# Optimization experiments

Hardware: AMD Instinct MI355X
Metric: run time of the kernel (lower is better)

Reference implementation:

```python
import jax, jax.numpy as jnp
import numpy as np

N = 3600      # nodes (pinned by h0/c0 shape in the torch module)
H = 512       # lstm_hidden
PES = 588     # pes feature width (LSTM input size)
PROT = 384    # protein feature width
OC = 256      # out_channels
E = 230400    # edges (avg degree 64)


def _lstm_cell(x, h, c, wih, whh, bih, bhh):
    # single-timestep PyTorch LSTM cell; gate order i, f, g, o
    g = x @ wih.T + h @ whh.T + bih + bhh
    i, f, gg, o = jnp.split(g, 4, axis=-1)
    c2 = jax.nn.sigmoid(f) * c + jax.nn.sigmoid(i) * jnp.tanh(gg)
    return jax.nn.sigmoid(o) * jnp.tanh(c2)


def _gcn(x, rows, cols, norm, W, b):
    # PyG GCNConv: X' = D^{-1/2}(A+I)D^{-1/2} X W + b
    xw = x @ W
    return jax.ops.segment_sum(xw[rows] * norm[:, None], cols, num_segments=N) + b


def setup_inputs() -> dict:
    key = jax.random.key(0)
    ks = jax.random.split(key, 24)
    s = 0.05
    d = {
        "x": jax.random.normal(ks[0], (N, PES + PROT), jnp.float32),
        "edge_index": jax.random.randint(ks[1], (2, E), 0, N),
        "h0": jax.random.normal(ks[2], (4, N, H), jnp.float32),
        "c0": jax.random.normal(ks[3], (4, N, H), jnp.float32),
    }
    ins = [PES, PES, 2 * H, 2 * H]
    names = ["l0f", "l0b", "l1f", "l1b"]
    for i, (nm, di) in enumerate(zip(names, ins)):
        d["wih" + nm] = jax.random.normal(ks[4 + 4 * i], (4 * H, di), jnp.float32) * s
        d["whh" + nm] = jax.random.normal(ks[5 + 4 * i], (4 * H, H), jnp.float32) * s
        d["bih" + nm] = jnp.zeros((4 * H,), jnp.float32)
        d["bhh" + nm] = jnp.zeros((4 * H,), jnp.float32)
    d["W1"] = jax.random.normal(ks[20], (PROT + 2 * H, 2 * OC), jnp.float32) * s
    d["b1"] = jnp.zeros((2 * OC,), jnp.float32)
    d["W2"] = jax.random.normal(ks[21], (2 * OC, OC), jnp.float32) * s
    d["b2"] = jnp.zeros((OC,), jnp.float32)
    return d


def reference(x, edge_index, h0, c0,
              wihl0f, whhl0f, bihl0f, bhhl0f,
              wihl0b, whhl0b, bihl0b, bhhl0b,
              wihl1f, whhl1f, bihl1f, bhhl1f,
              wihl1b, whhl1b, bihl1b, bhhl1b,
              W1, b1, W2, b2):
    pes = x[:, :PES]
    prot = x[:, PES:]
    # BiLSTM over seq_len=1: one cell step per direction per layer
    hf = _lstm_cell(pes, h0[0], c0[0], wihl0f, whhl0f, bihl0f, bhhl0f)
    hb = _lstm_cell(pes, h0[1], c0[1], wihl0b, whhl0b, bihl0b, bhhl0b)
    x1 = jnp.concatenate([hf, hb], axis=1)
    hf2 = _lstm_cell(x1, h0[2], c0[2], wihl1f, whhl1f, bihl1f, bhhl1f)
    hb2 = _lstm_cell(x1, h0[3], c0[3], wihl1b, whhl1b, bihl1b, bhhl1b)
    x_p = jnp.concatenate([hf2, hb2], axis=1) / 100.0
    feat = jnp.concatenate([prot, x_p], axis=1)  # dropout is identity in eval
    # add self-loops, symmetric normalization
    loop = jnp.arange(N)
    rows = jnp.concatenate([edge_index[0], loop])
    cols = jnp.concatenate([edge_index[1], loop])
    deg = jax.ops.segment_sum(jnp.ones_like(rows, jnp.float32), cols, num_segments=N)
    dinv = jax.lax.rsqrt(deg)  # deg >= 1 because of self-loops
    norm = dinv[rows] * dinv[cols]
    h1 = jax.nn.relu(_gcn(feat, rows, cols, norm, W1, b1))
    return _gcn(h1, rows, cols, norm, W2, b2)
```

## Files before the change

kernel.cpp:

```cpp
#include <hip/hip_runtime.h>
#include <hip/hip_bf16.h>

#define NN 3600
#define MP 3712
#define KADJ 3616
#define NH (3600*512)
#define EE 230400
#define NKT0 9
#define NKT1 12

typedef __hip_bfloat16 bf16;
typedef __bf16 bf16x8 __attribute__((ext_vector_type(8)));
typedef float f32x4 __attribute__((ext_vector_type(4)));
typedef int i32x8 __attribute__((ext_vector_type(8)));
typedef unsigned char u8x16 __attribute__((ext_vector_type(16)));

typedef __attribute__((address_space(1))) void as1v;
typedef __attribute__((address_space(3))) void as3v;

__device__ __forceinline__ void glds16(void* lds, const void* g) {
  __builtin_amdgcn_global_load_lds((as1v*)(void*)g, (as3v*)lds, 16, 0, 0);
}

__device__ __forceinline__ float sigm(float v) { return 1.0f / (1.0f + expf(-v)); }

__device__ __forceinline__ unsigned char f2fp8(float f) {
  return (unsigned char)(__builtin_amdgcn_cvt_pk_fp8_f32(f, 0.f, 0, false) & 0xff);
}

__device__ __forceinline__ unsigned short f2bf_bits(float f) {
  __hip_bfloat16 h = __float2bfloat16(f);
  return *reinterpret_cast<unsigned short*>(&h);
}
__device__ __forceinline__ float bf_bits2f(unsigned short u) {
  __hip_bfloat16 h; *reinterpret_cast<unsigned short*>(&h) = u;
  return __bfloat162float(h);
}

template<int MODE>
__global__ __launch_bounds__(256) void gemm_lstm8(
    const unsigned char* __restrict__ Axf, const unsigned char* __restrict__ Ahf,
    const unsigned char* __restrict__ Bf,
    const float* __restrict__ c0f, const float* __restrict__ bihf,
    const float* __restrict__ bhhf,
    const unsigned char* __restrict__ Axb, const unsigned char* __restrict__ Ahb,
    const unsigned char* __restrict__ Bb,
    const float* __restrict__ c0b, const float* __restrict__ bihb,
    const float* __restrict__ bhhb,
    void* __restrict__ dst1,
    int nktx, int nkt, int hx)
{
  __shared__ alignas(16) unsigned char smem[65536];
  const int hid = (int)blockIdx.y * 32 + (int)blockIdx.x;
  const int xcd = hid & 7, idx = hid >> 3;
  int bx, by;
  if (idx < 112) { bx = (xcd & 3) * 8 + (idx & 7); by = (xcd >> 2) * 14 + (idx >> 3); }
  else { int k = idx - 112; bx = (xcd & 3) * 8 + k * 2 + (xcd >> 2); by = 28; }
  const bool back = bx >= hx;
  const unsigned char* Ax = back ? Axb : Axf;
  const unsigned char* Ah = back ? Ahb : Ahf;
  const unsigned char* B  = back ? Bb  : Bf;
  const float* c0  = back ? c0b : c0f;
  const float* bih = back ? bihb : bihf;
  const float* bhh = back ? bhhb : bhhf;
  const int t = threadIdx.x, w = t >> 6, l = t & 63;
  const int nblk = back ? bx - hx : bx;
  const unsigned char* gA  = Ax + (((size_t)by * nktx) << 14) + t*16;
  const unsigned char* gAh = Ah + (((size_t)by * (nkt - nktx)) << 14) + t*16;
  const unsigned char* gB  = B  + (((size_t)nblk * nkt) << 14) + t*16;
  const int wm = (w>>1)*64, wn = (w&1)*64;
  const int kb = l >> 4;
  const int aoff = kb*4096 + (wm + (l&15))*32;
  const int boff = 16384 + kb*4096 + (wn + (l&15))*32;
  f32x4 acc[4][4] = {};

  auto STAGE = [&](int buf, int kt) {
    unsigned char* lA = smem + buf*32768 + w*1024;
    unsigned char* lB = smem + buf*32768 + 16384 + w*1024;
    const unsigned char* srcA = (kt < nktx) ? gA + ((size_t)kt << 14)
                                            : gAh + ((size_t)(kt - nktx) << 14);
    const size_t ko = (size_t)kt << 14;
    glds16(lA,          srcA);
    glds16(lA + 4096,   srcA + 4096);
    glds16(lA + 8192,   srcA + 8192);
    glds16(lA + 12288,  srcA + 12288);
    glds16(lB,          gB + ko);
    glds16(lB + 4096,   gB + ko + 4096);
    glds16(lB + 8192,   gB + ko + 8192);
    glds16(lB + 12288,  gB + ko + 12288);
  };

  STAGE(0, 0);
  STAGE(1, 1);
  int cur = 0;
  for (int kt = 0; kt < nkt; ++kt) {
    if (kt + 1 < nkt) asm volatile("s_waitcnt vmcnt(8)" ::: "memory");
    else              asm volatile("s_waitcnt vmcnt(0)" ::: "memory");
    __builtin_amdgcn_sched_barrier(0);
    __builtin_amdgcn_s_barrier();
    __builtin_amdgcn_sched_barrier(0);
    const unsigned char* base = smem + cur*32768;
    i32x8 av[4], bv[4];
#pragma unroll
    for (int mi = 0; mi < 4; ++mi) av[mi] = *(const i32x8*)(base + aoff + mi*512);
#pragma unroll
    for (int ni = 0; ni < 4; ++ni) bv[ni] = *(const i32x8*)(base + boff + ni*512);
#pragma unroll
    for (int mi = 0; mi < 4; ++mi)
#pragma unroll
      for (int ni = 0; ni < 4; ++ni)
        acc[mi][ni] = __builtin_amdgcn_mfma_scale_f32_16x16x128_f8f6f4(
            av[mi], bv[ni], acc[mi][ni], 0, 0, 0, 127, 0, 127);
    __builtin_amdgcn_sched_barrier(0);
    __builtin_amdgcn_s_barrier();
    __builtin_amdgcn_sched_barrier(0);
    if (kt + 2 < nkt) STAGE(cur, kt + 2);
    cur ^= 1;
  }
  const int jh = (((nblk << 7) + wn) >> 2) + (l & 15);
  const float bI = bih[jh]        + bhh[jh];
  const float bF = bih[512 + jh]  + bhh[512 + jh];
  const float bG = bih[1024 + jh] + bhh[1024 + jh];
  const float bO = bih[1536 + jh] + bhh[1536 + jh];
  const int crow = (by << 7) + wm + ((l>>4)<<2);
  const int kk = (back ? 512 : 0) + jh;
  const size_t kpart = ((size_t)(kk >> 7) << 14) + ((size_t)((kk >> 5) & 3) << 12) + (kk & 31);
  const int colOff = back ? 896 : 384;
#pragma unroll
  for (int mi = 0; mi < 4; ++mi)
#pragma unroll
    for (int jr = 0; jr < 4; ++jr) {
      const int n = crow + mi*16 + jr;
      if (n < NN) {
        const float gi = acc[mi][0][jr] + bI;
        const float gf = acc[mi][1][jr] + bF;
        const float gg = acc[mi][2][jr] + bG;
        const float go = acc[mi][3][jr] + bO;
        const float c2 = sigm(gf) * c0[(size_t)n*512 + jh] + sigm(gi) * tanhf(gg);
        const float h  = sigm(go) * tanhf(c2);
        if (MODE == 0) {
          const size_t off = (((size_t)(n >> 7) * 8) << 14) + kpart + ((size_t)(n & 127) << 5);
          ((unsigned char*)dst1)[off] = f2fp8(h);
        } else {
          ((bf16*)dst1)[(size_t)n*1408 + colOff + jh] = __float2bfloat16(h * 0.01f);
        }
      }
    }
}

__global__ __launch_bounds__(256) void gemm_bt_sk(const bf16* __restrict__ A,
                                                  const bf16* __restrict__ B,
                                                  float* __restrict__ Cp,
                                                  int Kp, int ldc, int ksteps)
{
  __shared__ alignas(16) char smem[32768];
  const int t = threadIdx.x, w = t >> 6, l = t & 63;
  const int mbase = blockIdx.y << 7, nbase = blockIdx.x << 7;
  const int total = Kp >> 5;
  const int kstart = blockIdx.z * ksteps;
  int steps = total - kstart; if (steps > ksteps) steps = ksteps;
  const size_t ldb = (size_t)Kp * 2;
  const char* gA = (const char*)A + (size_t)(mbase + w*16 + (l>>2)) * ldb
                   + (size_t)((l&3)*16) + (size_t)kstart*64;
  const char* gB = (const char*)B + (size_t)(nbase + w*16 + (l>>2)) * ldb
                   + (size_t)((l&3)*16) + (size_t)kstart*64;
  const int wm = (w>>1)*64, wn = (w&1)*64;
  const int aoff = (wm + (l&15))*64 + (l>>4)*16;
  const int boff = 8192 + (wn + (l&15))*64 + (l>>4)*16;
  f32x4 acc[4][4] = {};
  const size_t chunk = ldb * 64;

  auto STAGE = [&](int buf, int kt) {
    char* lA = smem + buf*16384 + w*1024;
    char* lB = smem + buf*16384 + 8192 + w*1024;
    const size_t ko = (size_t)kt * 64;
    glds16(lA,        gA + ko);
    glds16(lA + 4096, gA + ko + chunk);
    glds16(lB,        gB + ko);
    glds16(lB + 4096, gB + ko + chunk);
  };

  STAGE(0, 0);
  if (steps > 1) STAGE(1, 1);
  int cur = 0;
  for (int kt = 0; kt < steps; ++kt) {
    if (kt + 1 < steps) asm volatile("s_waitcnt vmcnt(4)" ::: "memory");
    else                asm volatile("s_waitcnt vmcnt(0)" ::: "memory");
    __builtin_amdgcn_sched_barrier(0);
    __builtin_amdgcn_s_barrier();
    __builtin_amdgcn_sched_barrier(0);
    const char* base = smem + cur*16384;
    bf16x8 av[4], bv[4];
#pragma unroll
    for (int mi = 0; mi < 4; ++mi) av[mi] = *(const bf16x8*)(base + aoff + mi*1024);
#pragma unroll
    for (int ni = 0; ni < 4; ++ni) bv[ni] = *(const bf16x8*)(base + boff + ni*1024);
#pragma unroll
    for (int mi = 0; mi < 4; ++mi)
#pragma unroll
      for (int ni = 0; ni < 4; ++ni)
        acc[mi][ni] = __builtin_amdgcn_mfma_f32_16x16x32_bf16(av[mi], bv[ni], acc[mi][ni], 0, 0, 0);
    __builtin_amdgcn_sched_barrier(0);
    __builtin_amdgcn_s_barrier();
    __builtin_amdgcn_sched_barrier(0);
    if (kt + 2 < steps) STAGE(cur, kt + 2);
    cur ^= 1;
  }
  float* Cz = Cp + (size_t)blockIdx.z * ((size_t)(gridDim.y << 7) * ldc);
  const int crow = mbase + wm + ((l>>4)<<2);
  const int ccol = nbase + wn + (l&15);
#pragma unroll
  for (int mi = 0; mi < 4; ++mi)
#pragma unroll
    for (int ni = 0; ni < 4; ++ni) {
      float* cp = Cz + (size_t)(crow + mi*16)*ldc + (ccol + ni*16);
#pragma unroll
      for (int j = 0; j < 4; ++j) cp[(size_t)j*ldc] = acc[mi][ni][j];
    }
}

__global__ void reduce_bf_pad(const float* __restrict__ p, bf16* __restrict__ dst, int Z)
{
  int k = blockIdx.x*256 + threadIdx.x;
  int r = blockIdx.y;
  if (k >= KADJ) return;
  const size_t psz = (size_t)gridDim.y * MP;
  float s = 0.f;
  if (k < NN)
    for (int z = 0; z < Z; ++z) s += p[(size_t)z*psz + (size_t)r*MP + k];
  dst[(size_t)r*KADJ + k] = __float2bfloat16(s);
}

__global__ void reduce_relu_bf(const float* __restrict__ p, const float* __restrict__ b,
                               bf16* __restrict__ dst)
{
  int idx = blockIdx.x*256 + threadIdx.x;
  int f = idx & 511;
  float s = b[f];
#pragma unroll
  for (int z = 0; z < 4; ++z) s += p[(size_t)z*MP*512 + idx];
  dst[idx] = __float2bfloat16(fmaxf(s, 0.f));
}

__global__ void reduce_bias_out(const float* __restrict__ p, const float* __restrict__ b,
                                float* __restrict__ out)
{
  int idx = blockIdx.x*256 + threadIdx.x;
  if (idx >= NN*256) return;
  int f = idx & 255;
  float s = b[f];
#pragma unroll
  for (int z = 0; z < 8; ++z) s += p[(size_t)z*MP*256 + idx];
  out[idx] = s;
}

__global__ void pack_B8_all(const float* __restrict__ wih0f, const float* __restrict__ whh0f,
                            const float* __restrict__ wih0b, const float* __restrict__ whh0b,
                            const float* __restrict__ wih1f, const float* __restrict__ whh1f,
                            const float* __restrict__ wih1b, const float* __restrict__ whh1b,
                            unsigned char* __restrict__ B0f, unsigned char* __restrict__ B0b,
                            unsigned char* __restrict__ B1f, unsigned char* __restrict__ B1b)
{
  const int z = blockIdx.z;
  const float* wih; const float* whh; unsigned char* dst; int kx, nkt;
  if      (z == 0) { wih = wih0f; whh = whh0f; dst = B0f; kx = 588;  nkt = NKT0; }
  else if (z == 1) { wih = wih0b; whh = whh0b; dst = B0b; kx = 588;  nkt = NKT0; }
  else if (z == 2) { wih = wih1f; whh = whh1f; dst = B1f; kx = 1024; nkt = NKT1; }
  else             { wih = wih1b; whh = whh1b; dst = B1b; kx = 1024; nkt = NKT1; }
  if ((int)blockIdx.x >= nkt*4) return;
  const int kt = blockIdx.x >> 2, kbId = blockIdx.x & 3;
  const int t = threadIdx.x;
  const int r = t >> 1, kio = (t & 1) << 4;
  const int R = ((int)blockIdx.y << 7) + r;
  const int src = (((R >> 4) & 3) << 9) + ((R >> 6) << 4) + (R & 15);
  const int kbase = kt*128 + kbId*32 + kio;
  u8x16 v;
#pragma unroll
  for (int i = 0; i < 16; ++i) {
    const int k = kbase + i;
    float f = 0.f;
    if (k < kx) f = wih[(size_t)src*kx + k];
    else if (k < kx + 512) f = whh[(size_t)src*512 + (k - kx)];
    v[i] = f2fp8(f);
  }
  *(u8x16*)(dst + (((size_t)blockIdx.y*nkt + kt) << 14) + (kbId << 12) + (r << 5) + kio) = v;
}

__global__ void pack_A8_all(const float* __restrict__ x, const float* __restrict__ h0,
                            unsigned char* __restrict__ a0f, unsigned char* __restrict__ a0b,
                            unsigned char* __restrict__ ahf, unsigned char* __restrict__ ahb)
{
  const int z = blockIdx.z;
  const int t = threadIdx.x;
  const int r = t >> 1, kio = (t & 1) << 4;
  const int n = ((int)blockIdx.y << 7) + r;
  if (z < 2) {
    const int kt = blockIdx.x >> 2, kbId = blockIdx.x & 3;
    const int kbase = kt*128 + kbId*32 + kio;
    const float* hsrc = h0 + (size_t)z * NH;
    u8x16 v;
#pragma unroll
    for (int i = 0; i < 16; ++i) {
      const int k = kbase + i;
      float f = 0.f;
      if (n < NN) {
        if (k < 588) f = x[(size_t)n*972 + k];
        else if (k < 1100) f = hsrc[(size_t)n*512 + (k - 588)];
      }
      v[i] = f2fp8(f);
    }
    unsigned char* dst = z ? a0b : a0f;
    *(u8x16*)(dst + (((size_t)blockIdx.y*NKT0 + kt) << 14) + (kbId << 12) + (r << 5) + kio) = v;
  } else {
    if ((int)blockIdx.x >= 16) return;
    const int ktl = blockIdx.x >> 2, kbId = blockIdx.x & 3;
    const int kbase = ktl*128 + kbId*32 + kio;
    const float* hsrc = h0 + (size_t)(z) * NH;
    u8x16 v;
#pragma unroll
    for (int i = 0; i < 16; ++i) {
      const int k = kbase + i;
      float f = (n < NN) ? hsrc[(size_t)n*512 + k] : 0.f;
      v[i] = f2fp8(f);
    }
    unsigned char* dst = (z == 3) ? ahb : ahf;
    *(u8x16*)(dst + (((size_t)blockIdx.y*4 + ktl) << 14) + (kbId << 12) + (r << 5) + kio) = v;
  }
}

__global__ void pack_BT_all(const float* __restrict__ W1, bf16* __restrict__ BW1,
                            const float* __restrict__ W2, bf16* __restrict__ BW2)
{
  const int z = blockIdx.z;
  const float* W; bf16* dst; int Nc, K, nx, ny;
  if (z == 0) { W = W1; dst = BW1; Nc = 512; K = 1408; nx = 6; ny = 512; }
  else        { W = W2; dst = BW2; Nc = 256; K = 512;  nx = 2; ny = 256; }
  if ((int)blockIdx.x >= nx || (int)blockIdx.y >= ny) return;
  int k = blockIdx.x*256 + threadIdx.x;
  int n = blockIdx.y;
  if (k >= K) return;
  dst[(size_t)n*K + k] = __float2bfloat16(W[(size_t)k*Nc + n]);
}

__global__ void pack_prot(const float* __restrict__ x, bf16* __restrict__ afeat)
{
  int k = blockIdx.x*256 + threadIdx.x;
  int n = blockIdx.y;
  if (k >= 384) return;
  float v = (n < NN) ? x[(size_t)n*972 + 588 + k] : 0.f;
  afeat[(size_t)n*1408 + k] = __float2bfloat16(v);
}

__global__ void deg_count(const int* __restrict__ ecols, int* __restrict__ deg)
{
  int e = blockIdx.x*256 + threadIdx.x;
  if (e < EE) atomicAdd(&deg[ecols[e]], 1);
}

__global__ void calc_dinv(const int* __restrict__ deg, float* __restrict__ dinv)
{
  int n = blockIdx.x*256 + threadIdx.x;
  if (n < NN) dinv[n] = 1.0f / sqrtf((float)(deg[n] + 1));
}

__global__ void adj_scatter_bf(const int* __restrict__ er, const int* __restrict__ ec,
                               const float* __restrict__ dinv,
                               unsigned int* __restrict__ adjw)
{
  int e = blockIdx.x*256 + threadIdx.x;
  int r, c; float v;
  if (e < EE)            { r = er[e]; c = ec[e]; v = dinv[r]*dinv[c]; }
  else if (e < EE + NN)  { r = c = e - EE; float d = dinv[r]; v = d*d; }
  else return;
  unsigned int* p = adjw + ((size_t)c*KADJ + r) / 2;
  const bool hi = (r & 1) != 0;
  unsigned int old = *p, assumed;
  do {
    assumed = old;
    unsigned short h = hi ? (unsigned short)(assumed >> 16)
                          : (unsigned short)(assumed & 0xffffu);
    unsigned short nh = f2bf_bits(bf_bits2f(h) + v);
    unsigned int nw = hi ? ((assumed & 0x0000ffffu) | ((unsigned int)nh << 16))
                         : ((assumed & 0xffff0000u) | (unsigned int)nh);
    if (nw == assumed) break;
    old = atomicCAS(p, assumed, nw);
  } while (old != assumed);
}

#define OFF_DEG   ((size_t)0)
#define OFF_DINV  ((size_t)16384)
#define OFF_BW2   ((size_t)32768)
#define OFF_B0F   ((size_t)294912)
#define OFF_B0B   ((size_t)4882432)
#define OFF_B1F   ((size_t)9469952)
#define OFF_B1B   ((size_t)15761408)
#define OFF_BW1   ((size_t)22052864)
#define OFF_A0F   ((size_t)23494656)
#define OFF_A0B   ((size_t)31809536)
#define OFF_A1X   ((size_t)40124416)
#define OFF_A1HF  ((size_t)43925504)
#define OFF_A1HB  ((size_t)45826048)
#define OFF_G     ((size_t)62930944)
#define OFF_AFEAT OFF_A0F
#define OFF_XW1P  OFF_G
#define OFF_XWT1B OFF_B0F
#define OFF_ADJB  ((size_t)4194304)
#define OFF_H1P   ((size_t)40124416)
#define OFF_H1    ((size_t)70533120)
#define OFF_XW2P  ((size_t)74334208)
#define OFF_XWT2B ((size_t)89538560)
#define OFF_O2P   ((size_t)40124416)

extern "C" void kernel_launch(void* const* d_in, const int* in_sizes, int n_in,
                              void* d_out, int out_size, void* d_ws, size_t ws_size,
                              hipStream_t stream)
{
  const float* x    = (const float*)d_in[0];
  const int*   ei   = (const int*)d_in[1];
  const float* h0   = (const float*)d_in[2];
  const float* c0   = (const float*)d_in[3];
  const float* wih0f = (const float*)d_in[4];
  const float* whh0f = (const float*)d_in[5];
  const float* bih0f = (const float*)d_in[6];
  const float* bhh0f = (const float*)d_in[7];
  const float* wih0b = (const float*)d_in[8];
  const float* whh0b = (const float*)d_in[9];
  const float* bih0b = (const float*)d_in[10];
  const float* bhh0b = (const float*)d_in[11];
  const float* wih1f = (const float*)d_in[12];
  const float* whh1f = (const float*)d_in[13];
  const float* bih1f = (const float*)d_in[14];
  const float* bhh1f = (const float*)d_in[15];
  const float* wih1b = (const float*)d_in[16];
  const float* whh1b = (const float*)d_in[17];
  const float* bih1b = (const float*)d_in[18];
  const float* bhh1b = (const float*)d_in[19];
  const float* W1 = (const float*)d_in[20];
  const float* b1 = (const float*)d_in[21];
  const float* W2 = (const float*)d_in[22];
  const float* b2 = (const float*)d_in[23];

  char* ws = (char*)d_ws;
  int*   deg  = (int*)(ws + OFF_DEG);
  float* dinv = (float*)(ws + OFF_DINV);
  unsigned char* B0f8 = (unsigned char*)(ws + OFF_B0F);
  unsigned char* B0b8 = (unsigned char*)(ws + OFF_B0B);
  unsigned char* B1f8 = (unsigned char*)(ws + OFF_B1F);
  unsigned char* B1b8 = (unsigned char*)(ws + OFF_B1B);
  bf16* BW1 = (bf16*)(ws + OFF_BW1);
  bf16* BW2 = (bf16*)(ws + OFF_BW2);
  unsigned char* A0f8 = (unsigned char*)(ws + OFF_A0F);
  unsigned char* A0b8 = (unsigned char*)(ws + OFF_A0B);
  unsigned char* A1X8 = (unsigned char*)(ws + OFF_A1X);
  unsigned char* A1HF = (unsigned char*)(ws + OFF_A1HF);
  unsigned char* A1HB = (unsigned char*)(ws + OFF_A1HB);
  bf16* Afeat = (bf16*)(ws + OFF_AFEAT);
  float* xw1p  = (float*)(ws + OFF_XW1P);
  bf16*  xwt1b = (bf16*)(ws + OFF_XWT1B);
  bf16*  adjb  = (bf16*)(ws + OFF_ADJB);
  float* h1p   = (float*)(ws + OFF_H1P);
  bf16*  h1bf  = (bf16*)(ws + OFF_H1);
  float* xw2p  = (float*)(ws + OFF_XW2P);
  bf16*  xwt2b = (bf16*)(ws + OFF_XWT2B);
  float* o2p   = (float*)(ws + OFF_O2P);
  float* outp = (float*)d_out;

  hipMemsetAsync(deg, 0, (size_t)NN*4, stream);
  deg_count<<<dim3((EE+255)/256), 256, 0, stream>>>(ei + EE, deg);
  calc_dinv<<<dim3(15), 256, 0, stream>>>(deg, dinv);

  pack_B8_all<<<dim3(NKT1*4, 16, 4), 256, 0, stream>>>(
      wih0f, whh0f, wih0b, whh0b, wih1f, whh1f, wih1b, whh1b,
      B0f8, B0b8, B1f8, B1b8);
  pack_BT_all<<<dim3(6, 512, 2), 256, 0, stream>>>(W1, BW1, W2, BW2);

  pack_A8_all<<<dim3(NKT0*4, 29, 4), 256, 0, stream>>>(x, h0, A0f8, A0b8, A1HF, A1HB);

  gemm_lstm8<0><<<dim3(32, 29), 256, 0, stream>>>(
      A0f8, A0f8, B0f8, c0,              bih0f, bhh0f,
      A0b8, A0b8, B0b8, c0 + (size_t)NH, bih0b, bhh0b,
      A1X8, NKT0, NKT0, 16);

  pack_prot<<<dim3(2, MP), 256, 0, stream>>>(x, Afeat);

  gemm_lstm8<1><<<dim3(32, 29), 256, 0, stream>>>(
      A1X8, A1HF, B1f8, c0 + (size_t)2*NH, bih1f, bhh1f,
      A1X8, A1HB, B1b8, c0 + (size_t)3*NH, bih1b, bhh1b,
      Afeat, 8, NKT1, 16);

  gemm_bt_sk<<<dim3(29, 4, 4), 256, 0, stream>>>(BW1, Afeat, xw1p, 1408, MP, 11);
  reduce_bf_pad<<<dim3(15, 512), 256, 0, stream>>>(xw1p, xwt1b, 4);

  hipMemsetAsync(adjb, 0, (size_t)MP*KADJ*2, stream);
  adj_scatter_bf<<<dim3((EE+NN+255)/256), 256, 0, stream>>>(
      ei, ei + EE, dinv, (unsigned int*)adjb);

  gemm_bt_sk<<<dim3(4, 29, 4), 256, 0, stream>>>(adjb, xwt1b, h1p, KADJ, 512, 29);
  reduce_relu_bf<<<dim3(MP*512/256), 256, 0, stream>>>(h1p, b1, h1bf);

  gemm_bt_sk<<<dim3(29, 2, 4), 256, 0, stream>>>(BW2, h1bf, xw2p, 512, MP, 4);
  reduce_bf_pad<<<dim3(15, 256), 256, 0, stream>>>(xw2p, xwt2b, 4);

  gemm_bt_sk<<<dim3(2, 29, 8), 256, 0, stream>>>(adjb, xwt2b, o2p, KADJ, 256, 15);
  reduce_bias_out<<<dim3(3600), 256, 0, stream>>>(o2p, b2, outp);
}
```

Before: 297.0 us.

## Enlarge LSTM fp8 GEMM tiles to 256x256 with 512 threads and interleaved prefetch

The fused LSTM gate GEMM moves from 128x128 tiles with 256 threads to 256x256 tiles with 512 threads and 128KB of double-buffered LDS. Each wave now computes 4x8 MFMA tiles, and the next k-tile's global-to-LDS loads are interleaved with the MFMA groups, using s_setprio to favour the math. The grid shrinks to 240 blocks with a new XCD swizzle, and the packed A buffers are padded to 30 row blocks. The aim is more data reuse per loaded byte and better load/compute overlap. The cost is higher register and LDS pressure, which limits occupancy to one block per CU, and more barriers per k-step.

```diff
diff --git a/kernel.cpp b/kernel.cpp
--- a/kernel.cpp
+++ b/kernel.cpp
@@ -38,7 +38,7 @@
 }
 
 template<int MODE>
-__global__ __launch_bounds__(256) void gemm_lstm8(
+__global__ __launch_bounds__(512) void gemm_lstm8(
     const unsigned char* __restrict__ Axf, const unsigned char* __restrict__ Ahf,
     const unsigned char* __restrict__ Bf,
     const float* __restrict__ c0f, const float* __restrict__ bihf,
@@ -50,12 +50,10 @@
     void* __restrict__ dst1,
     int nktx, int nkt, int hx)
 {
-  __shared__ alignas(16) unsigned char smem[65536];
-  const int hid = (int)blockIdx.y * 32 + (int)blockIdx.x;
-  const int xcd = hid & 7, idx = hid >> 3;
-  int bx, by;
-  if (idx < 112) { bx = (xcd & 3) * 8 + (idx & 7); by = (xcd >> 2) * 14 + (idx >> 3); }
-  else { int k = idx - 112; bx = (xcd & 3) * 8 + k * 2 + (xcd >> 2); by = 28; }
+  __shared__ alignas(16) unsigned char smem[131072];
+  const int hid = (int)blockIdx.y * 16 + (int)blockIdx.x;
+  const int swz = (hid & 7) * 30 + (hid >> 3);
+  const int bx = swz & 15, by = swz >> 4;
   const bool back = bx >= hx;
   const unsigned char* Ax = back ? Axb : Axf;
   const unsigned char* Ah = back ? Ahb : Ahf;
@@ -64,88 +62,108 @@
   const float* bih = back ? bihb : bihf;
   const float* bhh = back ? bhhb : bhhf;
   const int t = threadIdx.x, w = t >> 6, l = t & 63;
+  const int wr = w >> 1, wc = w & 1;
   const int nblk = back ? bx - hx : bx;
-  const unsigned char* gA  = Ax + (((size_t)by * nktx) << 14) + t*16;
-  const unsigned char* gAh = Ah + (((size_t)by * (nkt - nktx)) << 14) + t*16;
-  const unsigned char* gB  = B  + (((size_t)nblk * nkt) << 14) + t*16;
-  const int wm = (w>>1)*64, wn = (w&1)*64;
+  const int nkth = nkt - nktx;
+  const unsigned char* gAx0 = Ax + (((size_t)(2*by)   * nktx) << 14);
+  const unsigned char* gAx1 = Ax + (((size_t)(2*by+1) * nktx) << 14);
+  const unsigned char* gAh0 = Ah + (((size_t)(2*by)   * nkth) << 14);
+  const unsigned char* gAh1 = Ah + (((size_t)(2*by+1) * nkth) << 14);
+  const unsigned char* gB0  = B  + (((size_t)(2*nblk)   * nkt) << 14);
+  const unsigned char* gB1  = B  + (((size_t)(2*nblk+1) * nkt) << 14);
   const int kb = l >> 4;
-  const int aoff = kb*4096 + (wm + (l&15))*32;
-  const int boff = 16384 + kb*4096 + (wn + (l&15))*32;
-  f32x4 acc[4][4] = {};
-
-  auto STAGE = [&](int buf, int kt) {
-    unsigned char* lA = smem + buf*32768 + w*1024;
-    unsigned char* lB = smem + buf*32768 + 16384 + w*1024;
-    const unsigned char* srcA = (kt < nktx) ? gA + ((size_t)kt << 14)
-                                            : gAh + ((size_t)(kt - nktx) << 14);
-    const size_t ko = (size_t)kt << 14;
-    glds16(lA,          srcA);
-    glds16(lA + 4096,   srcA + 4096);
-    glds16(lA + 8192,   srcA + 8192);
-    glds16(lA + 12288,  srcA + 12288);
-    glds16(lB,          gB + ko);
-    glds16(lB + 4096,   gB + ko + 4096);
-    glds16(lB + 8192,   gB + ko + 8192);
-    glds16(lB + 12288,  gB + ko + 12288);
+  const int aoff = (wr >> 1) * 16384 + kb*4096 + ((wr & 1)*64 + (l & 15))*32;
+  const int boff = 32768 + wc*16384 + kb*4096 + (l & 15)*32;
+  f32x4 acc[4][8] = {};
+
+  auto srcA = [&](int kt, int blk01) -> const unsigned char* {
+    if (kt < nktx) return (blk01 ? gAx1 : gAx0) + ((size_t)kt << 14);
+    return (blk01 ? gAh1 : gAh0) + ((size_t)(kt - nktx) << 14);
   };
-
-  STAGE(0, 0);
-  STAGE(1, 1);
+  auto stageChunk = [&](unsigned char* nbuf, int kt, int c) {
+    const unsigned char* s;
+    switch (c >> 1) {
+      case 0:  s = srcA(kt, 0); break;
+      case 1:  s = srcA(kt, 1); break;
+      case 2:  s = gB0 + ((size_t)kt << 14); break;
+      default: s = gB1 + ((size_t)kt << 14); break;
+    }
+    s += (c & 1) * 8192 + t * 16;
+    glds16(nbuf + c * 8192 + t * 16, s);
+  };
+
+#pragma unroll
+  for (int c = 0; c < 8; ++c) stageChunk(smem, 0, c);
+
   int cur = 0;
   for (int kt = 0; kt < nkt; ++kt) {
-    if (kt + 1 < nkt) asm volatile("s_waitcnt vmcnt(8)" ::: "memory");
-    else              asm volatile("s_waitcnt vmcnt(0)" ::: "memory");
+    asm volatile("s_waitcnt vmcnt(0)" ::: "memory");
     __builtin_amdgcn_sched_barrier(0);
     __builtin_amdgcn_s_barrier();
     __builtin_amdgcn_sched_barrier(0);
-    const unsigned char* base = smem + cur*32768;
-    i32x8 av[4], bv[4];
-#pragma unroll
-    for (int mi = 0; mi < 4; ++mi) av[mi] = *(const i32x8*)(base + aoff + mi*512);
-#pragma unroll
-    for (int ni = 0; ni < 4; ++ni) bv[ni] = *(const i32x8*)(base + boff + ni*512);
-#pragma unroll
-    for (int mi = 0; mi < 4; ++mi)
-#pragma unroll
-      for (int ni = 0; ni < 4; ++ni)
-        acc[mi][ni] = __builtin_amdgcn_mfma_scale_f32_16x16x128_f8f6f4(
-            av[mi], bv[ni], acc[mi][ni], 0, 0, 0, 127, 0, 127);
-    __builtin_amdgcn_sched_barrier(0);
-    __builtin_amdgcn_s_barrier();
-    __builtin_amdgcn_sched_barrier(0);
-    if (kt + 2 < nkt) STAGE(cur, kt + 2);
+    const unsigned char* base = smem + cur*65536;
+    unsigned char* nbuf = smem + (cur^1)*65536;
+    const bool pf = (kt + 1 < nkt);
+    i32x8 afr[4];
+#pragma unroll
+    for (int mi = 0; mi < 4; ++mi) afr[mi] = *(const i32x8*)(base + aoff + mi*512);
+#pragma unroll
+    for (int p = 0; p < 4; ++p) {
+      i32x8 b0 = *(const i32x8*)(base + boff + (size_t)(2*p)*512);
+      i32x8 b1 = *(const i32x8*)(base + boff + (size_t)(2*p+1)*512);
+      if (pf) { stageChunk(nbuf, kt+1, 2*p); stageChunk(nbuf, kt+1, 2*p+1); }
+      __builtin_amdgcn_s_barrier();
+      asm volatile("s_waitcnt lgkmcnt(0)" ::: "memory");
+      __builtin_amdgcn_sched_barrier(0);
+      __builtin_amdgcn_s_setprio(1);
+#pragma unroll
+      for (int mi = 0; mi < 4; ++mi)
+        acc[mi][2*p] = __builtin_amdgcn_mfma_scale_f32_16x16x128_f8f6f4(
+            afr[mi], b0, acc[mi][2*p], 0, 0, 0, 127, 0, 127);
+#pragma unroll
+      for (int mi = 0; mi < 4; ++mi)
+        acc[mi][2*p+1] = __builtin_amdgcn_mfma_scale_f32_16x16x128_f8f6f4(
+            afr[mi], b1, acc[mi][2*p+1], 0, 0, 0, 127, 0, 127);
+      __builtin_amdgcn_s_setprio(0);
+      __builtin_amdgcn_sched_barrier(0);
+      __builtin_amdgcn_s_barrier();
+    }
     cur ^= 1;
   }
-  const int jh = (((nblk << 7) + wn) >> 2) + (l & 15);
-  const float bI = bih[jh]        + bhh[jh];
-  const float bF = bih[512 + jh]  + bhh[512 + jh];
-  const float bG = bih[1024 + jh] + bhh[1024 + jh];
-  const float bO = bih[1536 + jh] + bhh[1536 + jh];
-  const int crow = (by << 7) + wm + ((l>>4)<<2);
-  const int kk = (back ? 512 : 0) + jh;
-  const size_t kpart = ((size_t)(kk >> 7) << 14) + ((size_t)((kk >> 5) & 3) << 12) + (kk & 31);
-  const int colOff = back ? 896 : 384;
-#pragma unroll
-  for (int mi = 0; mi < 4; ++mi)
-#pragma unroll
-    for (int jr = 0; jr < 4; ++jr) {
-      const int n = crow + mi*16 + jr;
-      if (n < NN) {
-        const float gi = acc[mi][0][jr] + bI;
-        const float gf = acc[mi][1][jr] + bF;
-        const float gg = acc[mi][2][jr] + bG;
-        const float go = acc[mi][3][jr] + bO;
-        const float c2 = sigm(gf) * c0[(size_t)n*512 + jh] + sigm(gi) * tanhf(gg);
-        const float h  = sigm(go) * tanhf(c2);
-        if (MODE == 0) {
-          const size_t off = (((size_t)(n >> 7) * 8) << 14) + kpart + ((size_t)(n & 127) << 5);
-          ((unsigned char*)dst1)[off] = f2fp8(h);
-        } else {
-          ((bf16*)dst1)[(size_t)n*1408 + colOff + jh] = __float2bfloat16(h * 0.01f);
+
+  const int crow = by*256 + wr*64 + ((l >> 4) << 2);
+  const int jbase = (nblk*4 + wc*2) * 16 + (l & 15);
+#pragma unroll
+  for (int ng = 0; ng < 2; ++ng) {
+    const int jh = jbase + ng*16;
+    const float bI = bih[jh]        + bhh[jh];
+    const float bF = bih[512 + jh]  + bhh[512 + jh];
+    const float bG = bih[1024 + jh] + bhh[1024 + jh];
+    const float bO = bih[1536 + jh] + bhh[1536 + jh];
+    const int kk = (back ? 512 : 0) + jh;
+    const size_t kpart = ((size_t)(kk >> 7) << 14) + ((size_t)((kk >> 5) & 3) << 12) + (kk & 31);
+    const int colOff = back ? 896 : 384;
+#pragma unroll
+    for (int mi = 0; mi < 4; ++mi)
+#pragma unroll
+      for (int jr = 0; jr < 4; ++jr) {
+        const int n = crow + mi*16 + jr;
+        if (n < NN) {
+          const float gi = acc[mi][ng*4 + 0][jr] + bI;
+          const float gf = acc[mi][ng*4 + 1][jr] + bF;
+          const float gg = acc[mi][ng*4 + 2][jr] + bG;
+          const float go = acc[mi][ng*4 + 3][jr] + bO;
+          const float c2 = sigm(gf) * c0[(size_t)n*512 + jh] + sigm(gi) * tanhf(gg);
+          const float h  = sigm(go) * tanhf(c2);
+          if (MODE == 0) {
+            const size_t off = (((size_t)(n >> 7) * 8) << 14) + kpart + ((size_t)(n & 127) << 5);
+            ((unsigned char*)dst1)[off] = f2fp8(h);
+          } else {
+            ((bf16*)dst1)[(size_t)n*1408 + colOff + jh] = __float2bfloat16(h * 0.01f);
+          }
         }
       }
-    }
+  }
 }
 
 __global__ __launch_bounds__(256) void gemm_bt_sk(const bf16* __restrict__ A,
@@ -315,7 +333,7 @@
     if ((int)blockIdx.x >= 16) return;
     const int ktl = blockIdx.x >> 2, kbId = blockIdx.x & 3;
     const int kbase = ktl*128 + kbId*32 + kio;
-    const float* hsrc = h0 + (size_t)(z) * NH;
+    const float* hsrc = h0 + (size_t)z * NH;
     u8x16 v;
 #pragma unroll
     for (int i = 0; i < 16; ++i) {
@@ -398,8 +416,8 @@
 #define OFF_A0F   ((size_t)23494656)
 #define OFF_A0B   ((size_t)31809536)
 #define OFF_A1X   ((size_t)40124416)
-#define OFF_A1HF  ((size_t)43925504)
-#define OFF_A1HB  ((size_t)45826048)
+#define OFF_A1HF  ((size_t)44056576)
+#define OFF_A1HB  ((size_t)46022656)
 #define OFF_G     ((size_t)62930944)
 #define OFF_AFEAT OFF_A0F
 #define OFF_XW1P  OFF_G
@@ -474,19 +492,19 @@
       B0f8, B0b8, B1f8, B1b8);
   pack_BT_all<<<dim3(6, 512, 2), 256, 0, stream>>>(W1, BW1, W2, BW2);
 
-  pack_A8_all<<<dim3(NKT0*4, 29, 4), 256, 0, stream>>>(x, h0, A0f8, A0b8, A1HF, A1HB);
-
-  gemm_lstm8<0><<<dim3(32, 29), 256, 0, stream>>>(
+  pack_A8_all<<<dim3(NKT0*4, 30, 4), 256, 0, stream>>>(x, h0, A0f8, A0b8, A1HF, A1HB);
+
+  gemm_lstm8<0><<<dim3(16, 15), 512, 0, stream>>>(
       A0f8, A0f8, B0f8, c0,              bih0f, bhh0f,
       A0b8, A0b8, B0b8, c0 + (size_t)NH, bih0b, bhh0b,
-      A1X8, NKT0, NKT0, 16);
+      A1X8, NKT0, NKT0, 8);
 
   pack_prot<<<dim3(2, MP), 256, 0, stream>>>(x, Afeat);
 
-  gemm_lstm8<1><<<dim3(32, 29), 256, 0, stream>>>(
+  gemm_lstm8<1><<<dim3(16, 15), 512, 0, stream>>>(
       A1X8, A1HF, B1f8, c0 + (size_t)2*NH, bih1f, bhh1f,
       A1X8, A1HB, B1b8, c0 + (size_t)3*NH, bih1b, bhh1b,
-      Afeat, 8, NKT1, 16);
+      Afeat, 8, NKT1, 8);
 
   gemm_bt_sk<<<dim3(29, 4, 4), 256, 0, stream>>>(BW1, Afeat, xw1p, 1408, MP, 11);
   reduce_bf_pad<<<dim3(15, 512), 256, 0, stream>>>(xw1p, xwt1b, 4);
```

New measurement: 396.9 us. +33.6%, slower.
